# Optimization experiments

Measured on AMD Instinct MI355X. Metric: run time of the kernel, lower is better.

Reference implementation:

```python
import jax, jax.numpy as jnp
import numpy as np

EPS = 1e-5


def setup_inputs() -> dict:
    key = jax.random.key(0)
    ks = jax.random.split(key, 12)
    B, C, H, W = 1, 512, 64, 64
    d = C // 8
    inp = {
        "x": jax.random.normal(ks[0], (B, C, H, W), jnp.float32),
        "y": jax.random.normal(ks[1], (B, C, H, W), jnp.float32),
        "s_m": jax.random.uniform(ks[2], (H, W), jnp.float32),
        "q_m": jax.random.uniform(ks[3], (H, W), jnp.float32),
        "Wq": jax.random.normal(ks[4], (d, C), jnp.float32) * (1.0 / np.sqrt(C)),
        "bq": jnp.zeros((d,), jnp.float32),
        "Wk": jax.random.normal(ks[5], (d, C), jnp.float32) * (1.0 / np.sqrt(C)),
        "bk": jnp.zeros((d,), jnp.float32),
        "Wv": jax.random.normal(ks[6], (C, C), jnp.float32) * (1.0 / np.sqrt(C)),
        "bv": jnp.zeros((C,), jnp.float32),
        "W1": jax.random.normal(ks[7], (C, C), jnp.float32) * (1.0 / np.sqrt(C)),
        "b1": jnp.zeros((C,), jnp.float32),
        "W2": jax.random.normal(ks[8], (C, C), jnp.float32) * (1.0 / np.sqrt(C)),
        "b2": jnp.zeros((C,), jnp.float32),
        "gamma": jnp.ones((1, C, H, W), jnp.float32),
        "beta": jnp.zeros((1, C, H, W), jnp.float32),
    }
    return inp


def _conv1x1(x, Wt, b):
    # 1x1 Conv2d == per-pixel channel matmul
    return jnp.einsum("bchw,oc->bohw", x, Wt) + b[None, :, None, None]


def reference(x, y, s_m, q_m, Wq, bq, Wk, bk, Wv, bv, W1, b1, W2, b2, gamma, beta):
    B, C, H, W = x.shape
    N = H * W
    scale = (C // 8) ** (-0.5)

    q_m = jnp.where(q_m > 0.8, 1.0, 0.0).astype(x.dtype)
    x_fg = x * s_m[None, None]
    y_fg = y * q_m[None, None]

    def branch(q_in, k_in, v_in, use_max):
        q = _conv1x1(q_in, Wq, bq).reshape(B, -1, N).transpose(0, 2, 1) * scale  # [B,N,d]
        k = _conv1x1(k_in, Wk, bk).reshape(B, -1, N)                             # [B,d,N]
        v = _conv1x1(v_in, Wv, bv).reshape(B, -1, N)                             # [B,C,N]
        attn = jnp.einsum("bqd,bdk->bqk", q, k)                                  # [B,N,N]
        stat = jnp.max(attn) if use_max else jnp.min(attn)
        thr = (stat + jnp.mean(attn)) * 0.5
        attn = jnp.where(attn < thr, jnp.asarray(-999.0, attn.dtype), attn)
        attn = jax.nn.softmax(attn, axis=-1)
        out = jnp.einsum("bck,bqk->bcq", v, attn).reshape(B, C, H, W)
        h = out.transpose(0, 2, 3, 1)                                            # [B,H,W,C]
        h = jnp.maximum(h @ W1.T + b1, 0.0) @ W2.T + b2
        out = h.transpose(0, 3, 1, 2)
        # LayerNorm over all trailing dims [1,C,H,W] (B==1)
        mu = jnp.mean(out)
        var = jnp.mean((out - mu) ** 2)
        out = (out - mu) * jax.lax.rsqrt(var + EPS) * gamma + beta
        return out

    outx = branch(x_fg, y_fg, y_fg, True)
    outx = outx * s_m[None, None] + x * (1.0 - s_m)[None, None]
    outy = branch(y_fg, x, x, False)
    outy = outy * q_m[None, None] + y * (1.0 - q_m)[None, None]
    return outx, outy
```

## Files before the change

### kernel.cpp

```cpp
#include <hip/hip_runtime.h>
#include <math.h>

#define C_DIM 512
#define N_DIM 4096
#define CN (C_DIM * N_DIM)
#define SZO (N_DIM * C_DIM)
#define NN ((size_t)N_DIM * N_DIM)
#define NN_TOT ((long long)N_DIM * N_DIM)

typedef __attribute__((ext_vector_type(4))) float f32x4;
typedef __attribute__((ext_vector_type(8))) short short8;

__device__ __forceinline__ ushort f2bf(float f) {
    unsigned u = __float_as_uint(f);
    unsigned r = u + 0x7FFFu + ((u >> 16) & 1u);
    return (ushort)(r >> 16);
}
__device__ __forceinline__ float bf2f(ushort h) {
    return __uint_as_float((unsigned)h << 16);
}

__device__ __forceinline__ void gload16(const void* g, void* l) {
    __builtin_amdgcn_global_load_lds(
        (const __attribute__((address_space(1))) void*)g,
        (__attribute__((address_space(3))) void*)l, 16, 0, 0);
}

__global__ __launch_bounds__(256) void tconv64(
    const float* __restrict__ x, const float* __restrict__ y,
    ushort* __restrict__ xbT, ushort* __restrict__ ybT)
{
    const float* X = blockIdx.z ? y : x;
    ushort* XT = blockIdx.z ? ybT : xbT;
    __shared__ float t[64][65];
    const int c0 = blockIdx.x * 64;
    const int r0 = blockIdx.y * 64;
    const int ty = threadIdx.x >> 4, tx = threadIdx.x & 15;
    #pragma unroll
    for (int i = 0; i < 4; ++i) {
        int r = ty + i * 16;
        float4 v = *(const float4*)&X[(size_t)(r0 + r) * N_DIM + c0 + tx * 4];
        t[r][tx * 4 + 0] = v.x; t[r][tx * 4 + 1] = v.y;
        t[r][tx * 4 + 2] = v.z; t[r][tx * 4 + 3] = v.w;
    }
    __syncthreads();
    #pragma unroll
    for (int i = 0; i < 4; ++i) {
        int nn = ty + i * 16;
        ushort4 o;
        o.x = f2bf(t[tx * 4 + 0][nn]); o.y = f2bf(t[tx * 4 + 1][nn]);
        o.z = f2bf(t[tx * 4 + 2][nn]); o.w = f2bf(t[tx * 4 + 3][nn]);
        *(ushort4*)&XT[(size_t)(c0 + nn) * C_DIM + r0 + tx * 4] = o;
    }
}

__global__ __launch_bounds__(256) void cvtw3(
    const float* __restrict__ Wv, const float* __restrict__ W1,
    const float* __restrict__ W2, ushort* __restrict__ Wvb,
    ushort* __restrict__ W1b, ushort* __restrict__ W2b)
{
    const float* in  = (blockIdx.y == 0) ? Wv : (blockIdx.y == 1) ? W1 : W2;
    ushort*      out = (blockIdx.y == 0) ? Wvb : (blockIdx.y == 1) ? W1b : W2b;
    int i = (blockIdx.x * 256 + threadIdx.x) * 4;
    float4 v = *(const float4*)&in[i];
    ushort4 o = { f2bf(v.x), f2bf(v.y), f2bf(v.z), f2bf(v.w) };
    *(ushort4*)&out[i] = o;
}

template<int BM, int BN>
__global__ __launch_bounds__(256) void mfma_g(
    const ushort* __restrict__ A0, const ushort* __restrict__ A1,
    const ushort* __restrict__ B0, const ushort* __restrict__ B1,
    void* __restrict__ Out, size_t outBrStride,
    int M, int N, int K, int kLen, int nkz, int swapxy,
    const float* __restrict__ bias, int biasMode,
    const float* __restrict__ mask0, int mm0,
    const float* __restrict__ mask1, int mm1,
    int doRelu, int outBf16, float* __restrict__ lnp)
{
    constexpr int WAVES_M = BM / 64;
    constexpr int WAVES_N = 4 / WAVES_M;
    constexpr int WN = BN / WAVES_N;
    constexpr int FM = 4;
    constexpr int FN = WN / 16;
    constexpr int NCHUNK = (BM + BN) / 16;

    __shared__ ushort As[2][BM * 32];
    __shared__ ushort Bs[2][BN * 32];
    const int tid  = threadIdx.x;
    const int lane = tid & 63;
    const int wid  = tid >> 6;
    const int z  = blockIdx.z;
    const int br = z / nkz;
    const int kz = z % nkz;
    const ushort* A = br ? A1 : A0;
    const ushort* B = br ? B1 : B0;
    const float* mask = br ? mask1 : mask0;
    const int maskMode = br ? mm1 : mm0;

    const int bxm = swapxy ? blockIdx.x : blockIdx.y;
    const int bxn = swapxy ? blockIdx.y : blockIdx.x;
    const int m0 = bxm * BM, n0 = bxn * BN;
    const int wm = wid / WAVES_N, wn = wid % WAVES_N;
    const int wr = wm * 64, wc = wn * WN;
    const int kOff = kz * kLen;
    const int lrow = lane >> 2;
    const int kbl  = lane & 3;

    auto stage = [&](int buf, int t) {
        #pragma unroll
        for (int c = wid; c < NCHUNK; c += 4) {
            if (c < BM / 16) {
                int r = c * 16 + lrow;
                int kb = kbl ^ ((r >> 1) & 3);
                gload16(A + (size_t)(m0 + r) * K + kOff + t * 32 + kb * 8,
                        &As[buf][c * 512]);
            } else {
                int cb = c - BM / 16;
                int r = cb * 16 + lrow;
// ... 48 lines not shown
            for (int nc = 0; nc < FN; ++nc)
                #pragma unroll
                for (int j = 0; j < 4; ++j) {
                    int gm = m0 + wr + mr * 16 + orow + j;
                    int gn = n0 + wc + nc * 16 + ocol;
                    Of[(size_t)gm * N + gn] = acc[mr][nc][j];
                }
        return;
    }

    float mcol[FN], bcol[FN];
    #pragma unroll
    for (int nc = 0; nc < FN; ++nc) {
        int gn = n0 + wc + nc * 16 + ocol;
        mcol[nc] = (maskMode == 0) ? 1.0f
                 : (maskMode == 1) ? mask[gn]
                                   : (mask[gn] > 0.8f ? 1.0f : 0.0f);
        bcol[nc] = (biasMode == 2) ? bias[gn] : 0.0f;
    }
    ushort* Obf = (ushort*)Out + (size_t)br * outBrStride;
    float*  Of  = (float*)Out + (size_t)br * outBrStride;
    float lsum = 0.0f, lsq = 0.0f;
    #pragma unroll
    for (int mr = 0; mr < FM; ++mr) {
        #pragma unroll
        for (int j = 0; j < 4; ++j) {
            int gm = m0 + wr + mr * 16 + orow + j;
            float brow = (biasMode == 1) ? bias[gm] : 0.0f;
            #pragma unroll
            for (int nc = 0; nc < FN; ++nc) {
                int gn = n0 + wc + nc * 16 + ocol;
                float v = acc[mr][nc][j] * mcol[nc] + brow + bcol[nc];
                if (doRelu) v = fmaxf(v, 0.0f);
                if (outBf16) Obf[(size_t)gm * N + gn] = f2bf(v);
                else         Of[(size_t)gm * N + gn] = v;
                lsum += v; lsq = fmaf(v, v, lsq);
            }
        }
    }
    if (lnp) {
        __shared__ float redS[256], redQ[256];
        redS[tid] = lsum; redQ[tid] = lsq;
        __syncthreads();
        for (int s = 128; s > 0; s >>= 1) {
            if (tid < s) { redS[tid] += redS[tid + s]; redQ[tid] += redQ[tid + s]; }
            __syncthreads();
        }
        if (tid == 0) {
            int fb = blockIdx.y * gridDim.x + blockIdx.x;
            lnp[br * 512 + fb] = redS[0];
            lnp[br * 512 + 256 + fb] = redQ[0];
        }
    }
}

__global__ __launch_bounds__(256) void qkraw(
    const float* __restrict__ Wq, const float* __restrict__ Wk,
    const float* __restrict__ x, const float* __restrict__ y,
    float* __restrict__ PX)
{
    const int mt   = blockIdx.y & 1;
    const int srcT = blockIdx.y >> 1;
    const int kz   = blockIdx.z;
    const float* W = mt ? Wk : Wq;
    const float* X = srcT ? y : x;

    __shared__ float As[16][65];
    __shared__ float Bs[16][65];
    const int tid = threadIdx.x;
    const int n0 = blockIdx.x * 64;
    const int ty = tid >> 4, tx = tid & 15;
    float acc[4][4] = {};
    const int kbase = kz * 256;

    for (int k0 = kbase; k0 < kbase + 256; k0 += 16) {
        {
            int mm = tid >> 2, kq = (tid & 3) * 4;
            const float4 w4 = *(const float4*)&W[(size_t)mm * 512 + k0 + kq];
            As[kq + 0][mm] = w4.x; As[kq + 1][mm] = w4.y;
            As[kq + 2][mm] = w4.z; As[kq + 3][mm] = w4.w;
        }
        {
            int kk = tid >> 4, nq = (tid & 15) * 4;
            *(float4*)&Bs[kk][nq] = *(const float4*)&X[(size_t)(k0 + kk) * N_DIM + n0 + nq];
        }
        __syncthreads();
        #pragma unroll
        for (int kk = 0; kk < 16; ++kk) {
            float a[4], b[4];
            #pragma unroll
            for (int r = 0; r < 4; ++r) a[r] = As[kk][ty * 4 + r];
            #pragma unroll
            for (int c = 0; c < 4; ++c) b[c] = Bs[kk][tx * 4 + c];
            #pragma unroll
            for (int r = 0; r < 4; ++r)
                #pragma unroll
                for (int c = 0; c < 4; ++c)
                    acc[r][c] = fmaf(a[r], b[c], acc[r][c]);
        }
        __syncthreads();
    }
    float* dst = PX + ((size_t)(kz * 2 + srcT) * 128 + mt * 64) * N_DIM;
    #pragma unroll
    for (int r = 0; r < 4; ++r) {
        float4 o = make_float4(acc[r][0], acc[r][1], acc[r][2], acc[r][3]);
        *(float4*)&dst[(size_t)(ty * 4 + r) * N_DIM + n0 + tx * 4] = o;
    }
}

__global__ __launch_bounds__(256) void qkfinish(
    const float* __restrict__ PX,
    const float* __restrict__ s_m, const float* __restrict__ q_m,
    const float* __restrict__ bq, const float* __restrict__ bk,
    ushort* __restrict__ QF0, ushort* __restrict__ KF0,
    ushort* __restrict__ QF1, ushort* __restrict__ KF1)
{
    int gid = blockIdx.x * 256 + threadIdx.x;
    int lane = gid & 63;
    int rest = gid >> 6;
    int blk = rest & 255;
    int tensor = rest >> 8;
    int fr = lane & 15, quad = lane >> 4;
    int n = blk * 16 + fr;

    int srcT, rowbase, isQ;
    const float* bias;
    ushort* dst;
    float mv, scale;
    if (tensor == 0)      { srcT = 0; rowbase = 0;  isQ = 1; bias = bq; dst = QF0; scale = 0.125f; mv = s_m[n]; }
    else if (tensor == 1) { srcT = 1; rowbase = 64; isQ = 0; bias = bk; dst = KF0; scale = 1.0f;   mv = (q_m[n] > 0.8f) ? 1.0f : 0.0f; }
    else if (tensor == 2) { srcT = 1; rowbase = 0;  isQ = 1; bias = bq; dst = QF1; scale = 0.125f; mv = (q_m[n] > 0.8f) ? 1.0f : 0.0f; }
    else                  { srcT = 0; rowbase = 64; isQ = 0; bias = bk; dst = KF1; scale = 1.0f;   mv = 1.0f; }

    ushort hi0[8], lo0[8], hi1[8], lo1[8];
    #pragma unroll
    for (int j = 0; j < 8; ++j) {
        int d0 = quad * 8 + j, d1 = 32 + d0;
        float v0 = 0.0f, v1 = 0.0f;
        #pragma unroll
        for (int kz = 0; kz < 2; ++kz) {
            size_t base = ((size_t)(kz * 2 + srcT) * 128 + rowbase);
            v0 += PX[(base + d0) * N_DIM + n];
            v1 += PX[(base + d1) * N_DIM + n];
        }
        v0 = (v0 * mv + bias[d0]) * scale;
        v1 = (v1 * mv + bias[d1]) * scale;
        hi0[j] = f2bf(v0); lo0[j] = f2bf(v0 - bf2f(hi0[j]));
        hi1[j] = f2bf(v1); lo1[j] = f2bf(v1 - bf2f(hi1[j]));
    }
    auto wr8 = [&](int kstep, const ushort* v) {
        size_t base = ((size_t)(blk * 6 + kstep) * 64 + lane) * 8;
        *(ushort4*)&dst[base]     = *(const ushort4*)&v[0];
        *(ushort4*)&dst[base + 4] = *(const ushort4*)&v[4];
    };
    wr8(0, hi0); wr8(1, hi1);
    if (isQ) { wr8(2, hi0); wr8(3, hi1); wr8(4, lo0); wr8(5, lo1); }
    else     { wr8(2, lo0); wr8(3, lo1); wr8(4, hi0); wr8(5, hi1); }
}

__device__ __forceinline__ void scores_mfma(
    const ushort* __restrict__ QF, const ushort* __restrict__ KF,
    int m0, int n0, int wr, int wc, int lane, f32x4 acc[4][4])
{
    const int blkA0 = (m0 + wr) >> 4;
    const int blkB0 = (n0 + wc) >> 4;
    #pragma unroll
    for (int s = 0; s < 6; ++s) {
        short8 af[4], bf[4];
        #pragma unroll
        for (int mr = 0; mr < 4; ++mr)
            af[mr] = *(const short8*)&QF[((size_t)((blkA0 + mr) * 6 + s) * 64 + lane) * 8];
        #pragma unroll
        for (int nc = 0; nc < 4; ++nc)
            bf[nc] = *(const short8*)&KF[((size_t)((blkB0 + nc) * 6 + s) * 64 + lane) * 8];
        #pragma unroll
        for (int mr = 0; mr < 4; ++mr)
            #pragma unroll
            for (int nc = 0; nc < 4; ++nc)
                acc[mr][nc] = __builtin_amdgcn_mfma_f32_16x16x32_bf16(
                    af[mr], bf[nc], acc[mr][nc], 0, 0, 0);
    }
}

__global__ __launch_bounds__(256) void scores_pass1(
    const ushort* __restrict__ QF0, const ushort* __restrict__ KF0,
    const ushort* __restrict__ QF1, const ushort* __restrict__ KF1,
    float* __restrict__ part, float* __restrict__ rowmaxp)
{
    const int br = blockIdx.z;
    const ushort* QF = br ? QF1 : QF0;
    const ushort* KF = br ? KF1 : KF0;
    part    += (size_t)br * 3072;
    rowmaxp += (size_t)br * 131072;

    const int lane = threadIdx.x & 63, wid = threadIdx.x >> 6;
    const int m0 = blockIdx.y * 128, n0 = blockIdx.x * 128;
    const int wr = (wid >> 1) * 64, wc = (wid & 1) * 64;
    f32x4 acc[4][4] = {};
    scores_mfma(QF, KF, m0, n0, wr, wc, lane, acc);

    float lmax = -3.4e38f, lmin = 3.4e38f, lsum = 0.0f;
    float rmx[4][4];
    #pragma unroll
    for (int mr = 0; mr < 4; ++mr)
        #pragma unroll
        for (int j = 0; j < 4; ++j) rmx[mr][j] = -3.4e38f;
    #pragma unroll
    for (int mr = 0; mr < 4; ++mr)
        #pragma unroll
        for (int nc = 0; nc < 4; ++nc)
            #pragma unroll
            for (int j = 0; j < 4; ++j) {
                float v = acc[mr][nc][j];
                lsum += v; lmax = fmaxf(lmax, v); lmin = fminf(lmin, v);
                rmx[mr][j] = fmaxf(rmx[mr][j], v);
            }
    #pragma unroll
    for (int m = 1; m < 16; m <<= 1)
        #pragma unroll
        for (int mr = 0; mr < 4; ++mr)
            #pragma unroll
            for (int j = 0; j < 4; ++j)
                rmx[mr][j] = fmaxf(rmx[mr][j], __shfl_xor(rmx[mr][j], m, 64));

    __shared__ float wrm[2][128];
    const int orow = (lane >> 4) * 4;
    if ((lane & 15) == 0) {
        #pragma unroll
        for (int mr = 0; mr < 4; ++mr)
            #pragma unroll
            for (int j = 0; j < 4; ++j)
                wrm[wid & 1][wr + mr * 16 + orow + j] = rmx[mr][j];
    }
    __syncthreads();
    if (threadIdx.x < 128) {
        float v = fmaxf(wrm[0][threadIdx.x], wrm[1][threadIdx.x]);
        rowmaxp[(size_t)blockIdx.x * 4096 + m0 + threadIdx.x] = v;
    }

    __shared__ float red[256];
    const int tid = threadIdx.x;
    const int bid = blockIdx.y * 32 + blockIdx.x;
    __syncthreads();
    red[tid] = lmax; __syncthreads();
    for (int s = 128; s > 0; s >>= 1) { if (tid < s) red[tid] = fmaxf(red[tid], red[tid + s]); __syncthreads(); }
    if (tid == 0) part[bid] = red[0];
    __syncthreads();
    red[tid] = lmin; __syncthreads();
    for (int s = 128; s > 0; s >>= 1) { if (tid < s) red[tid] = fminf(red[tid], red[tid + s]); __syncthreads(); }
    if (tid == 0) part[1024 + bid] = red[0];
    __syncthreads();
    red[tid] = lsum; __syncthreads();
    for (int s = 128; s > 0; s >>= 1) { if (tid < s) red[tid] += red[tid + s]; __syncthreads(); }
    if (tid == 0) part[2048 + bid] = red[0];
}

__global__ __launch_bounds__(256) void stats_fin2(
    const float* __restrict__ part, float* __restrict__ stats)
{
    const int br = blockIdx.x;
    part += (size_t)br * 3072;
    __shared__ float rmax[256], rmin[256];
    __shared__ double rsum[256];
    int tid = threadIdx.x;
    float m1 = -3.4e38f, m2 = 3.4e38f; double s = 0.0;
    for (int i = tid; i < 1024; i += 256) {
        m1 = fmaxf(m1, part[i]);
        m2 = fminf(m2, part[1024 + i]);
        s += (double)part[2048 + i];
    }
    rmax[tid] = m1; rmin[tid] = m2; rsum[tid] = s;
    __syncthreads();
    for (int st = 128; st > 0; st >>= 1) {
        if (tid < st) {
            rmax[tid] = fmaxf(rmax[tid], rmax[tid + st]);
            rmin[tid] = fminf(rmin[tid], rmin[tid + st]);
            rsum[tid] += rsum[tid + st];
        }
        __syncthreads();
    }
    if (tid == 0) {
        float stat = (br == 0) ? rmax[0] : rmin[0];
        float mean = (float)(rsum[0] / (double)NN_TOT);
        stats[br] = 0.5f * (stat + mean);
    }
}

__global__ __launch_bounds__(256) void scores_pass2(
    const ushort* __restrict__ QF0, const ushort* __restrict__ KF0,
    const ushort* __restrict__ QF1, const ushort* __restrict__ KF1,
    const float* __restrict__ stats, const float* __restrict__ rowmaxp,
    ushort* __restrict__ Pe, float* __restrict__ rowsump)
{
    const int br = blockIdx.z;
    const ushort* QF = br ? QF1 : QF0;
    const ushort* KF = br ? KF1 : KF0;
    ushort* P = Pe + (size_t)br * NN;
    rowsump += (size_t)br * 131072;
    rowmaxp += (size_t)br * 131072;

    const int lane = threadIdx.x & 63, wid = threadIdx.x >> 6;
    const int m0 = blockIdx.y * 128, n0 = blockIdx.x * 128;
    const int wr = (wid >> 1) * 64, wc = (wid & 1) * 64;
    const float thr = stats[br];

    __shared__ float rowmL[128];
    if (threadIdx.x < 128) {
        int r = m0 + threadIdx.x;
        float m = -3.4e38f;
        #pragma unroll 8
        for (int b = 0; b < 32; ++b)
            m = fmaxf(m, rowmaxp[(size_t)b * 4096 + r]);
        rowmL[threadIdx.x] = (m >= thr) ? m : -1e30f;
    }
    __syncthreads();

    f32x4 acc[4][4] = {};
    scores_mfma(QF, KF, m0, n0, wr, wc, lane, acc);

    const int orow = (lane >> 4) * 4;
    const int ocol = lane & 15;
    float rm[4][4], rs[4][4];
    #pragma unroll
    for (int mr = 0; mr < 4; ++mr)
        #pragma unroll
        for (int j = 0; j < 4; ++j) {
            rm[mr][j] = rowmL[wr + mr * 16 + orow + j];
            rs[mr][j] = 0.0f;
        }
    #pragma unroll
    for (int mr = 0; mr < 4; ++mr)
        #pragma unroll
        for (int nc = 0; nc < 4; ++nc)
            #pragma unroll
            for (int j = 0; j < 4; ++j) {
                float s = acc[mr][nc][j];
                float m = rm[mr][j];
                float e = (s < thr) ? 0.0f : __expf(s - m);
                if (m < -1e29f) e = 1.0f;
                ushort h = f2bf(e);
                rs[mr][j] += bf2f(h);
                P[(size_t)(m0 + wr + mr * 16 + orow + j) * N_DIM
                  + n0 + wc + nc * 16 + ocol] = h;
            }
    #pragma unroll
    for (int m = 1; m < 16; m <<= 1)
        #pragma unroll
        for (int mr = 0; mr < 4; ++mr)
            #pragma unroll
            for (int j = 0; j < 4; ++j)
                rs[mr][j] += __shfl_xor(rs[mr][j], m, 64);

    __shared__ float wrs[2][128];
    if ((lane & 15) == 0) {
        #pragma unroll
        for (int mr = 0; mr < 4; ++mr)
            #pragma unroll
            for (int j = 0; j < 4; ++j)
                wrs[wid & 1][wr + mr * 16 + orow + j] = rs[mr][j];
    }
    __syncthreads();
    if (threadIdx.x < 128)
        rowsump[(size_t)blockIdx.x * 4096 + m0 + threadIdx.x] =
            wrs[0][threadIdx.x] + wrs[1][threadIdx.x];
}

__global__ __launch_bounds__(256) void reduce2row(
    const float* __restrict__ P4, const float* __restrict__ rowsump,
    ushort* __restrict__ O)
{
    const int br = blockIdx.y;
    const int tid = threadIdx.x;
    const int r0 = blockIdx.x * 2;
    __shared__ float invL[2];
    if (tid < 64) {
        int rw = tid >> 5, b = tid & 31;
        float s = rowsump[(size_t)br * 131072 + (size_t)b * 4096 + r0 + rw];
        #pragma unroll
        for (int m = 1; m < 32; m <<= 1) s += __shfl_xor(s, m, 64);
        if (b == 0) invL[rw] = 1.0f / s;
    }
    __syncthreads();
    int i = (blockIdx.x * 256 + tid) * 4;
    float sc = invL[(i >> 9) & 1];
    float4 a = *(const float4*)&P4[(size_t)(br * 2 + 0) * SZO + i];
    float4 b = *(const float4*)&P4[(size_t)(br * 2 + 1) * SZO + i];
    ushort4 o;
    o.x = f2bf((a.x + b.x) * sc);
    o.y = f2bf((a.y + b.y) * sc);
    o.z = f2bf((a.z + b.z) * sc);
    o.w = f2bf((a.w + b.w) * sc);
    *(ushort4*)&O[(size_t)br * SZO + i] = o;
}

__global__ __launch_bounds__(256) void gate_write(
    const float* __restrict__ H2, const float* __restrict__ lnp,
    const float* __restrict__ gamma, const float* __restrict__ beta,
    const float* __restrict__ x, const float* __restrict__ y,
    const float* __restrict__ s_m, const float* __restrict__ q_m,
    float* __restrict__ out)
{
    const int br = blockIdx.y;
    const int tid = threadIdx.x;
    __shared__ double rs[256], rq[256];
    rs[tid] = (double)lnp[(size_t)br * 512 + tid];
    rq[tid] = (double)lnp[(size_t)br * 512 + 256 + tid];
    __syncthreads();
    for (int st = 128; st > 0; st >>= 1) {
        if (tid < st) { rs[tid] += rs[tid + st]; rq[tid] += rq[tid + st]; }
        __syncthreads();
    }
    double muD = rs[0] / (double)CN;
    double varD = rq[0] / (double)CN - muD * muD;
    float mu = (float)muD;
    float rstd = (float)(1.0 / sqrt(varD + 1e-5));

    size_t i = ((size_t)blockIdx.x * 256 + tid) * 4;
// ... 16 lines not shown
    }
    float4 o; o.x = os[0]; o.y = os[1]; o.z = os[2]; o.w = os[3];
    *(float4*)&out[(size_t)br * CN + i] = o;
}

extern "C" void kernel_launch(void* const* d_in, const int* in_sizes, int n_in,
                              void* d_out, int out_size, void* d_ws, size_t ws_size,
                              hipStream_t stream)
{
    const float* x     = (const float*)d_in[0];
    const float* y     = (const float*)d_in[1];
    const float* s_m   = (const float*)d_in[2];
    const float* q_m   = (const float*)d_in[3];
    const float* Wq    = (const float*)d_in[4];
    const float* bq    = (const float*)d_in[5];
    const float* Wk    = (const float*)d_in[6];
    const float* bk    = (const float*)d_in[7];
    const float* Wv    = (const float*)d_in[8];
    const float* bv    = (const float*)d_in[9];
    const float* W1    = (const float*)d_in[10];
    const float* b1    = (const float*)d_in[11];
    const float* W2    = (const float*)d_in[12];
    const float* b2    = (const float*)d_in[13];
    const float* gamma = (const float*)d_in[14];
    const float* beta  = (const float*)d_in[15];
    float* out = (float*)d_out;

    float* ws = (float*)d_ws;
    float*  R1    = ws;
    float*  PX    = R1;
    float*  P4    = R1;
    ushort* QF0   = (ushort*)(R1 + 4194304);
    ushort* KF0   = QF0 + 786432;
    ushort* QF1   = KF0 + 786432;
    ushort* KF1   = QF1 + 786432;
    float*  SMALL = R1 + 8388608;
    float*  PART  = SMALL;
    float*  RMAXP = PART + 6144;
    float*  RSUMP = RMAXP + 262144;
    float*  LNP   = RSUMP + 262144;
    float*  STATS = LNP + 1024;
    ushort* Wvb   = (ushort*)(STATS + 64);
    ushort* W1b   = Wvb + 262144;
    ushort* W2b   = W1b + 262144;
    ushort* Vb    = W2b + 262144;
    ushort* R2    = Vb + 4194304;
    ushort* xbT   = R2;
    ushort* ybT   = R2 + 2097152;
    ushort* Pe    = R2;
    ushort* O1T   = R2;
    ushort* H1T   = R2 + 4194304;
    float*  H2    = (float*)(R2 + 8388608);

    tconv64<<<dim3(64, 8, 2), 256, 0, stream>>>(x, y, xbT, ybT);
    cvtw3<<<dim3(256, 3), 256, 0, stream>>>(Wv, W1, W2, Wvb, W1b, W2b);

    qkraw<<<dim3(64, 4, 2), 256, 0, stream>>>(Wq, Wk, x, y, PX);
    qkfinish<<<256, 256, 0, stream>>>(PX, s_m, q_m, bq, bk, QF0, KF0, QF1, KF1);

    mfma_g<64, 128><<<dim3(32, 8, 2), 256, 0, stream>>>(
        Wvb, Wvb, ybT, xbT, Vb, (size_t)CN,
        512, 4096, 512, 512, 1, 0, bv, 1, q_m, 2, nullptr, 0, 0, 1, nullptr);

    scores_pass1<<<dim3(32, 32, 2), 256, 0, stream>>>(QF0, KF0, QF1, KF1, PART, RMAXP);
    stats_fin2<<<2, 256, 0, stream>>>(PART, STATS);
    scores_pass2<<<dim3(32, 32, 2), 256, 0, stream>>>(QF0, KF0, QF1, KF1, STATS, RMAXP, Pe, RSUMP);

    mfma_g<64, 128><<<dim3(64, 4, 4), 256, 0, stream>>>(
        Pe, Pe + NN, Vb, Vb + CN, P4, 0,
        4096, 512, 4096, 2048, 2, 1, nullptr, 0, nullptr, 0, nullptr, 0, 0, 0, nullptr);
    reduce2row<<<dim3(2048, 2), 256, 0, stream>>>(P4, RSUMP, O1T);

    mfma_g<64, 64><<<dim3(64, 8, 2), 256, 0, stream>>>(
        O1T, O1T + SZO, W1b, W1b, H1T, (size_t)SZO,
        4096, 512, 512, 512, 1, 1, b1, 2, nullptr, 0, nullptr, 0, 1, 1, nullptr);

    mfma_g<64, 128><<<dim3(32, 8, 2), 256, 0, stream>>>(
        W2b, W2b, H1T, H1T + SZO, H2, (size_t)CN,
        512, 4096, 512, 512, 1, 0, b2, 1, nullptr, 0, nullptr, 0, 0, 0, LNP);

    gate_write<<<dim3(2048, 2), 256, 0, stream>>>(
        H2, LNP, gamma, beta, x, y, s_m, q_m, out);
}
```

Measured before the change: 255.9 us.

## Merge setup and projection kernels, fold stats reduction into pass2, enlarge GEMM tiles

Combines the transpose/convert, weight conversion and Q/K projection into one launch, with Q and K computed together so each x tile is loaded once. Fuses the V projection GEMM with scores pass1 in a single heterogeneous grid. Drops the separate stats kernel, so every pass2 block recomputes the global threshold from the partials. Raises the P·V and first FFN GEMM tiles to 128 rows. The goal is fewer launches, less idle tail time between small kernels and more reuse per tile. In exchange, pass2 blocks repeat the stats reduction and the bigger tiles yield fewer blocks.

```diff
diff --git a/kernel.cpp b/kernel.cpp
--- a/kernel.cpp
+++ b/kernel.cpp
@@ -26,45 +26,458 @@
         (__attribute__((address_space(3))) void*)l, 16, 0, 0);
 }
 
-__global__ __launch_bounds__(256) void tconv64(
+__global__ __launch_bounds__(256) void setup_all(
     const float* __restrict__ x, const float* __restrict__ y,
-    ushort* __restrict__ xbT, ushort* __restrict__ ybT)
-{
-    const float* X = blockIdx.z ? y : x;
-    ushort* XT = blockIdx.z ? ybT : xbT;
-    __shared__ float t[64][65];
-    const int c0 = blockIdx.x * 64;
-    const int r0 = blockIdx.y * 64;
-    const int ty = threadIdx.x >> 4, tx = threadIdx.x & 15;
-    #pragma unroll
-    for (int i = 0; i < 4; ++i) {
-        int r = ty + i * 16;
-        float4 v = *(const float4*)&X[(size_t)(r0 + r) * N_DIM + c0 + tx * 4];
-        t[r][tx * 4 + 0] = v.x; t[r][tx * 4 + 1] = v.y;
-        t[r][tx * 4 + 2] = v.z; t[r][tx * 4 + 3] = v.w;
-    }
-    __syncthreads();
-    #pragma unroll
-    for (int i = 0; i < 4; ++i) {
-        int nn = ty + i * 16;
-        ushort4 o;
-        o.x = f2bf(t[tx * 4 + 0][nn]); o.y = f2bf(t[tx * 4 + 1][nn]);
-        o.z = f2bf(t[tx * 4 + 2][nn]); o.w = f2bf(t[tx * 4 + 3][nn]);
-        *(ushort4*)&XT[(size_t)(c0 + nn) * C_DIM + r0 + tx * 4] = o;
-    }
-}
-
-__global__ __launch_bounds__(256) void cvtw3(
+    ushort* __restrict__ xbT, ushort* __restrict__ ybT,
     const float* __restrict__ Wv, const float* __restrict__ W1,
     const float* __restrict__ W2, ushort* __restrict__ Wvb,
-    ushort* __restrict__ W1b, ushort* __restrict__ W2b)
-{
-    const float* in  = (blockIdx.y == 0) ? Wv : (blockIdx.y == 1) ? W1 : W2;
-    ushort*      out = (blockIdx.y == 0) ? Wvb : (blockIdx.y == 1) ? W1b : W2b;
-    int i = (blockIdx.x * 256 + threadIdx.x) * 4;
-    float4 v = *(const float4*)&in[i];
-    ushort4 o = { f2bf(v.x), f2bf(v.y), f2bf(v.z), f2bf(v.w) };
-    *(ushort4*)&out[i] = o;
+    ushort* __restrict__ W1b, ushort* __restrict__ W2b,
+    const float* __restrict__ Wq, const float* __restrict__ Wk,
+    float* __restrict__ PX)
+{
+    __shared__ float t[64][65];
+    __shared__ float Asw[16][130];
+    __shared__ float Bsx[16][65];
+    const int id = blockIdx.x;
+    const int tid = threadIdx.x;
+
+    if (id < 1024) {
+        const int bx = id & 63, by = (id >> 6) & 7, bz = id >> 9;
+        const float* X = bz ? y : x;
+        ushort* XT = bz ? ybT : xbT;
+        const int c0 = bx * 64, r0 = by * 64;
+        const int ty = tid >> 4, tx = tid & 15;
+        #pragma unroll
+        for (int i = 0; i < 4; ++i) {
+            int r = ty + i * 16;
+            float4 v = *(const float4*)&X[(size_t)(r0 + r) * N_DIM + c0 + tx * 4];
+            t[r][tx * 4 + 0] = v.x; t[r][tx * 4 + 1] = v.y;
+            t[r][tx * 4 + 2] = v.z; t[r][tx * 4 + 3] = v.w;
+        }
+        __syncthreads();
+        #pragma unroll
+        for (int i = 0; i < 4; ++i) {
+            int nn = ty + i * 16;
+            ushort4 o;
+            o.x = f2bf(t[tx * 4 + 0][nn]); o.y = f2bf(t[tx * 4 + 1][nn]);
+            o.z = f2bf(t[tx * 4 + 2][nn]); o.w = f2bf(t[tx * 4 + 3][nn]);
+            *(ushort4*)&XT[(size_t)(c0 + nn) * C_DIM + r0 + tx * 4] = o;
+        }
+        return;
+    }
+    if (id < 1792) {
+        const int i2 = id - 1024;
+        const int bx = i2 & 255, by = i2 >> 8;
+        const float* in  = (by == 0) ? Wv : (by == 1) ? W1 : W2;
+        ushort*      out = (by == 0) ? Wvb : (by == 1) ? W1b : W2b;
+        int i = (bx * 256 + tid) * 4;
+        float4 v = *(const float4*)&in[i];
+        ushort4 o = { f2bf(v.x), f2bf(v.y), f2bf(v.z), f2bf(v.w) };
+        *(ushort4*)&out[i] = o;
+        return;
+    }
+    {
+        const int i3 = id - 1792;
+        const int ntile = i3 & 63;
+        const int srcT  = (i3 >> 6) & 1;
+        const int kz    = i3 >> 7;
+        const float* X = srcT ? y : x;
+        const int n0 = ntile * 64;
+        const int ty = tid >> 4, tx = tid & 15;
+        float accQ[4][4] = {}, accK[4][4] = {};
+        const int kbase = kz * 256;
+
+        for (int k0 = kbase; k0 < kbase + 256; k0 += 16) {
+            #pragma unroll
+            for (int i = 0; i < 2; ++i) {
+                int wi = tid + i * 256;
+                int mm = wi >> 2;
+                int kq = (wi & 3) * 4;
+                const float* Wp = (mm < 64) ? &Wq[(size_t)mm * 512]
+                                            : &Wk[(size_t)(mm - 64) * 512];
+                float4 w4 = *(const float4*)&Wp[k0 + kq];
+                Asw[kq + 0][mm] = w4.x; Asw[kq + 1][mm] = w4.y;
+                Asw[kq + 2][mm] = w4.z; Asw[kq + 3][mm] = w4.w;
+            }
+            {
+                int kk = tid >> 4, nq = (tid & 15) * 4;
+                *(float4*)&Bsx[kk][nq] = *(const float4*)&X[(size_t)(k0 + kk) * N_DIM + n0 + nq];
+            }
+            __syncthreads();
+            #pragma unroll
+            for (int kk = 0; kk < 16; ++kk) {
+                float aq[4], ak[4], b[4];
+                #pragma unroll
+                for (int r = 0; r < 4; ++r) { aq[r] = Asw[kk][ty * 4 + r]; ak[r] = Asw[kk][64 + ty * 4 + r]; }
+                #pragma unroll
+                for (int c = 0; c < 4; ++c) b[c] = Bsx[kk][tx * 4 + c];
+                #pragma unroll
+                for (int r = 0; r < 4; ++r)
+                    #pragma unroll
+                    for (int c = 0; c < 4; ++c) {
+                        accQ[r][c] = fmaf(aq[r], b[c], accQ[r][c]);
+                        accK[r][c] = fmaf(ak[r], b[c], accK[r][c]);
+                    }
+            }
+            __syncthreads();
+        }
+        float* dst = PX + ((size_t)(kz * 2 + srcT) * 128) * N_DIM;
+        #pragma unroll
+        for (int r = 0; r < 4; ++r) {
+            float4 oq = make_float4(accQ[r][0], accQ[r][1], accQ[r][2], accQ[r][3]);
+            *(float4*)&dst[(size_t)(ty * 4 + r) * N_DIM + n0 + tx * 4] = oq;
+            float4 ok = make_float4(accK[r][0], accK[r][1], accK[r][2], accK[r][3]);
+            *(float4*)&dst[(size_t)(64 + ty * 4 + r) * N_DIM + n0 + tx * 4] = ok;
+        }
+    }
+}
+
+__global__ __launch_bounds__(256) void qkfinish(
+    const float* __restrict__ PX,
+    const float* __restrict__ s_m, const float* __restrict__ q_m,
+    const float* __restrict__ bq, const float* __restrict__ bk,
+    ushort* __restrict__ QF0, ushort* __restrict__ KF0,
+    ushort* __restrict__ QF1, ushort* __restrict__ KF1)
+{
+    int gid = blockIdx.x * 256 + threadIdx.x;
+    int lane = gid & 63;
+    int rest = gid >> 6;
+    int blk = rest & 255;
+    int tensor = rest >> 8;
+    int fr = lane & 15, quad = lane >> 4;
+    int n = blk * 16 + fr;
+
+    int srcT, rowbase, isQ;
+    const float* bias;
+    ushort* dst;
+    float mv, scale;
+    if (tensor == 0)      { srcT = 0; rowbase = 0;  isQ = 1; bias = bq; dst = QF0; scale = 0.125f; mv = s_m[n]; }
+    else if (tensor == 1) { srcT = 1; rowbase = 64; isQ = 0; bias = bk; dst = KF0; scale = 1.0f;   mv = (q_m[n] > 0.8f) ? 1.0f : 0.0f; }
+    else if (tensor == 2) { srcT = 1; rowbase = 0;  isQ = 1; bias = bq; dst = QF1; scale = 0.125f; mv = (q_m[n] > 0.8f) ? 1.0f : 0.0f; }
+    else                  { srcT = 0; rowbase = 64; isQ = 0; bias = bk; dst = KF1; scale = 1.0f;   mv = 1.0f; }
+
+    ushort hi0[8], lo0[8], hi1[8], lo1[8];
+    #pragma unroll
+    for (int j = 0; j < 8; ++j) {
+        int d0 = quad * 8 + j, d1 = 32 + d0;
+        float v0 = 0.0f, v1 = 0.0f;
+        #pragma unroll
+        for (int kz = 0; kz < 2; ++kz) {
+            size_t base = ((size_t)(kz * 2 + srcT) * 128 + rowbase);
+            v0 += PX[(base + d0) * N_DIM + n];
+            v1 += PX[(base + d1) * N_DIM + n];
+        }
+        v0 = (v0 * mv + bias[d0]) * scale;
+        v1 = (v1 * mv + bias[d1]) * scale;
+        hi0[j] = f2bf(v0); lo0[j] = f2bf(v0 - bf2f(hi0[j]));
+        hi1[j] = f2bf(v1); lo1[j] = f2bf(v1 - bf2f(hi1[j]));
+    }
+    auto wr8 = [&](int kstep, const ushort* v) {
+        size_t base = ((size_t)(blk * 6 + kstep) * 64 + lane) * 8;
+        *(ushort4*)&dst[base]     = *(const ushort4*)&v[0];
+        *(ushort4*)&dst[base + 4] = *(const ushort4*)&v[4];
+    };
+    wr8(0, hi0); wr8(1, hi1);
+    if (isQ) { wr8(2, hi0); wr8(3, hi1); wr8(4, lo0); wr8(5, lo1); }
+    else     { wr8(2, lo0); wr8(3, lo1); wr8(4, hi0); wr8(5, hi1); }
+}
+
+__device__ __forceinline__ void scores_mfma(
+    const ushort* __restrict__ QF, const ushort* __restrict__ KF,
+    int m0, int n0, int wr, int wc, int lane, f32x4 acc[4][4])
+{
+    const int blkA0 = (m0 + wr) >> 4;
+    const int blkB0 = (n0 + wc) >> 4;
+    #pragma unroll
+    for (int s = 0; s < 6; ++s) {
+        short8 af[4], bf[4];
+        #pragma unroll
+        for (int mr = 0; mr < 4; ++mr)
+            af[mr] = *(const short8*)&QF[((size_t)((blkA0 + mr) * 6 + s) * 64 + lane) * 8];
+        #pragma unroll
+        for (int nc = 0; nc < 4; ++nc)
+            bf[nc] = *(const short8*)&KF[((size_t)((blkB0 + nc) * 6 + s) * 64 + lane) * 8];
+        #pragma unroll
+        for (int mr = 0; mr < 4; ++mr)
+            #pragma unroll
+            for (int nc = 0; nc < 4; ++nc)
+                acc[mr][nc] = __builtin_amdgcn_mfma_f32_16x16x32_bf16(
+                    af[mr], bf[nc], acc[mr][nc], 0, 0, 0);
+    }
+}
+
+__global__ __launch_bounds__(256) void vproj_p1(
+    const ushort* __restrict__ Wvb,
+    const ushort* __restrict__ xbT, const ushort* __restrict__ ybT,
+    const float* __restrict__ bv, const float* __restrict__ q_m,
+    ushort* __restrict__ Vb,
+    const ushort* __restrict__ QF0, const ushort* __restrict__ KF0,
+    const ushort* __restrict__ QF1, const ushort* __restrict__ KF1,
+    float* __restrict__ part, float* __restrict__ rowmaxp)
+{
+    __shared__ ushort As[2][128 * 32];
+    __shared__ ushort Bs[2][128 * 32];
+    __shared__ float wrm[2][128];
+    __shared__ float red[256];
+    const int id = blockIdx.x;
+    const int tid = threadIdx.x;
+    const int lane = tid & 63;
+    const int wid  = tid >> 6;
+
+    if (id < 256) {
+        const int bxn = id & 31;
+        const int bym = (id >> 5) & 3;
+        const int br  = id >> 7;
+        const ushort* A = Wvb;
+        const ushort* B = br ? xbT : ybT;
+        const int m0 = bym * 128, n0 = bxn * 128;
+        const int wr = (wid >> 1) * 64, wc = (wid & 1) * 64;
+        const int lrow = lane >> 2;
+        const int kbl  = lane & 3;
+        const int K = 512;
+
+        auto stage = [&](int buf, int t) {
+            #pragma unroll
+            for (int c = wid; c < 16; c += 4) {
+                if (c < 8) {
+                    int r = c * 16 + lrow;
+                    int kb = kbl ^ ((r >> 1) & 3);
+                    gload16(A + (size_t)(m0 + r) * K + t * 32 + kb * 8, &As[buf][c * 512]);
+                } else {
+                    int cb = c - 8;
+                    int r = cb * 16 + lrow;
+                    int kb = kbl ^ ((r >> 1) & 3);
+                    gload16(B + (size_t)(n0 + r) * K + t * 32 + kb * 8, &Bs[buf][cb * 512]);
+                }
+            }
+        };
+
+        f32x4 acc[4][4] = {};
+        const int fr = lane & 15;
+        const int kq = lane >> 4;
+        stage(0, 0);
+        asm volatile("s_waitcnt vmcnt(0)" ::: "memory");
+        __syncthreads();
+        int cur = 0;
+        for (int t = 0; t < 16; ++t) {
+            if (t + 1 < 16) stage(cur ^ 1, t + 1);
+            short8 af[4], bf[4];
+            #pragma unroll
+            for (int mr = 0; mr < 4; ++mr) {
+                int rA = wr + mr * 16 + fr;
+                af[mr] = *(const short8*)&As[cur][rA * 32 + (kq ^ ((rA >> 1) & 3)) * 8];
+            }
+            #pragma unroll
+            for (int nc = 0; nc < 4; ++nc) {
+                int rB = wc + nc * 16 + fr;
+                bf[nc] = *(const short8*)&Bs[cur][rB * 32 + (kq ^ ((rB >> 1) & 3)) * 8];
+            }
+            #pragma unroll
+            for (int mr = 0; mr < 4; ++mr)
+                #pragma unroll
+                for (int nc = 0; nc < 4; ++nc)
+                    acc[mr][nc] = __builtin_amdgcn_mfma_f32_16x16x32_bf16(
+                        af[mr], bf[nc], acc[mr][nc], 0, 0, 0);
+            asm volatile("s_waitcnt vmcnt(0)" ::: "memory");
+            __syncthreads();
+            cur ^= 1;
+        }
+        const int orow = (lane >> 4) * 4;
+        const int ocol = lane & 15;
+        float mcol[4];
+        #pragma unroll
+        for (int nc = 0; nc < 4; ++nc) {
+            int gn = n0 + wc + nc * 16 + ocol;
+            mcol[nc] = br ? 1.0f : ((q_m[gn] > 0.8f) ? 1.0f : 0.0f);
+        }
+        ushort* Obf = Vb + (size_t)br * CN;
+        #pragma unroll
+        for (int mr = 0; mr < 4; ++mr)
+            #pragma unroll
+            for (int j = 0; j < 4; ++j) {
+                int gm = m0 + wr + mr * 16 + orow + j;
+                float brow = bv[gm];
+                #pragma unroll
+                for (int nc = 0; nc < 4; ++nc) {
+                    int gn = n0 + wc + nc * 16 + ocol;
+                    float v = acc[mr][nc][j] * mcol[nc] + brow;
+                    Obf[(size_t)gm * N_DIM + gn] = f2bf(v);
+                }
+            }
+        return;
+    }
+
+    {
+        const int p = id - 256;
+        const int bxn = p & 31;
+        const int bym = (p >> 5) & 31;
+        const int br  = p >> 10;
+        const ushort* QF = br ? QF1 : QF0;
+        const ushort* KF = br ? KF1 : KF0;
+        float* pt = part + (size_t)br * 3072;
+        float* rmp = rowmaxp + (size_t)br * 131072;
+
+        const int m0 = bym * 128, n0 = bxn * 128;
+        const int wr = (wid >> 1) * 64, wc = (wid & 1) * 64;
+        f32x4 acc[4][4] = {};
+        scores_mfma(QF, KF, m0, n0, wr, wc, lane, acc);
+
+        float lmax = -3.4e38f, lmin = 3.4e38f, lsum = 0.0f;
+        float rmx[4][4];
+        #pragma unroll
+        for (int mr = 0; mr < 4; ++mr)
+            #pragma unroll
+            for (int j = 0; j < 4; ++j) rmx[mr][j] = -3.4e38f;
+        #pragma unroll
+        for (int mr = 0; mr < 4; ++mr)
+            #pragma unroll
+            for (int nc = 0; nc < 4; ++nc)
+                #pragma unroll
+                for (int j = 0; j < 4; ++j) {
+                    float v = acc[mr][nc][j];
+                    lsum += v; lmax = fmaxf(lmax, v); lmin = fminf(lmin, v);
+                    rmx[mr][j] = fmaxf(rmx[mr][j], v);
+                }
+        #pragma unroll
+        for (int m = 1; m < 16; m <<= 1)
+            #pragma unroll
+            for (int mr = 0; mr < 4; ++mr)
+                #pragma unroll
+                for (int j = 0; j < 4; ++j)
+                    rmx[mr][j] = fmaxf(rmx[mr][j], __shfl_xor(rmx[mr][j], m, 64));
+
+        const int orow = (lane >> 4) * 4;
+        if ((lane & 15) == 0) {
+            #pragma unroll
+            for (int mr = 0; mr < 4; ++mr)
+                #pragma unroll
+                for (int j = 0; j < 4; ++j)
+                    wrm[wid & 1][wr + mr * 16 + orow + j] = rmx[mr][j];
+        }
+        __syncthreads();
+        if (tid < 128) {
+            float v = fmaxf(wrm[0][tid], wrm[1][tid]);
+            rmp[(size_t)bxn * 4096 + m0 + tid] = v;
+        }
+
+        const int bid = bym * 32 + bxn;
+        __syncthreads();
+        red[tid] = lmax; __syncthreads();
+        for (int s = 128; s > 0; s >>= 1) { if (tid < s) red[tid] = fmaxf(red[tid], red[tid + s]); __syncthreads(); }
+        if (tid == 0) pt[bid] = red[0];
+        __syncthreads();
+        red[tid] = lmin; __syncthreads();
+        for (int s = 128; s > 0; s >>= 1) { if (tid < s) red[tid] = fminf(red[tid], red[tid + s]); __syncthreads(); }
+        if (tid == 0) pt[1024 + bid] = red[0];
+        __syncthreads();
+        red[tid] = lsum; __syncthreads();
+        for (int s = 128; s > 0; s >>= 1) { if (tid < s) red[tid] += red[tid + s]; __syncthreads(); }
+        if (tid == 0) pt[2048 + bid] = red[0];
+    }
+}
+
+__global__ __launch_bounds__(256) void scores_pass2(
+    const ushort* __restrict__ QF0, const ushort* __restrict__ KF0,
+    const ushort* __restrict__ QF1, const ushort* __restrict__ KF1,
+    const float* __restrict__ part, const float* __restrict__ rowmaxp,
+    ushort* __restrict__ Pe, float* __restrict__ rowsump)
+{
+    const int br = blockIdx.z;
+    const ushort* QF = br ? QF1 : QF0;
+    const ushort* KF = br ? KF1 : KF0;
+    ushort* P = Pe + (size_t)br * NN;
+    rowsump += (size_t)br * 131072;
+    rowmaxp += (size_t)br * 131072;
+    const float* pp = part + (size_t)br * 3072;
+
+    const int tid = threadIdx.x;
+    const int lane = tid & 63, wid = tid >> 6;
+    const int m0 = blockIdx.y * 128, n0 = blockIdx.x * 128;
+    const int wr = (wid >> 1) * 64, wc = (wid & 1) * 64;
+
+    __shared__ float smx[256], smn[256];
+    __shared__ double ssm[256];
+    {
+        float m1 = -3.4e38f, m2 = 3.4e38f; double s = 0.0;
+        for (int i = tid; i < 1024; i += 256) {
+            m1 = fmaxf(m1, pp[i]);
+            m2 = fminf(m2, pp[1024 + i]);
+            s += (double)pp[2048 + i];
+        }
+        smx[tid] = m1; smn[tid] = m2; ssm[tid] = s;
+        __syncthreads();
+        for (int st = 128; st > 0; st >>= 1) {
+            if (tid < st) {
+                smx[tid] = fmaxf(smx[tid], smx[tid + st]);
+                smn[tid] = fminf(smn[tid], smn[tid + st]);
+                ssm[tid] += ssm[tid + st];
+            }
+            __syncthreads();
+        }
+    }
+    const float stat = (br == 0) ? smx[0] : smn[0];
+    const float mean = (float)(ssm[0] / (double)NN_TOT);
+    const float thr = 0.5f * (stat + mean);
+
+    __shared__ float rowmL[128];
+    if (tid < 128) {
+        int r = m0 + tid;
+        float m = -3.4e38f;
+        #pragma unroll 8
+        for (int b = 0; b < 32; ++b)
+            m = fmaxf(m, rowmaxp[(size_t)b * 4096 + r]);
+        rowmL[tid] = (m >= thr) ? m : -1e30f;
+    }
+    __syncthreads();
+
+    f32x4 acc[4][4] = {};
+    scores_mfma(QF, KF, m0, n0, wr, wc, lane, acc);
+
+    const int orow = (lane >> 4) * 4;
+    const int ocol = lane & 15;
+    float rm[4][4], rs[4][4];
+    #pragma unroll
+    for (int mr = 0; mr < 4; ++mr)
+        #pragma unroll
+        for (int j = 0; j < 4; ++j) {
+            rm[mr][j] = rowmL[wr + mr * 16 + orow + j];
+            rs[mr][j] = 0.0f;
+        }
+    #pragma unroll
+    for (int mr = 0; mr < 4; ++mr)
+        #pragma unroll
+        for (int nc = 0; nc < 4; ++nc)
+            #pragma unroll
+            for (int j = 0; j < 4; ++j) {
+                float s = acc[mr][nc][j];
+                float m = rm[mr][j];
+                float e = (s < thr) ? 0.0f : __expf(s - m);
+                if (m < -1e29f) e = 1.0f;
+                ushort h = f2bf(e);
+                rs[mr][j] += bf2f(h);
+                P[(size_t)(m0 + wr + mr * 16 + orow + j) * N_DIM
+                  + n0 + wc + nc * 16 + ocol] = h;
+            }
+    #pragma unroll
+    for (int m = 1; m < 16; m <<= 1)
+        #pragma unroll
+        for (int mr = 0; mr < 4; ++mr)
+            #pragma unroll
+            for (int j = 0; j < 4; ++j)
+                rs[mr][j] += __shfl_xor(rs[mr][j], m, 64);
+
+    __shared__ float wrs[2][128];
+    if ((lane & 15) == 0) {
+        #pragma unroll
+        for (int mr = 0; mr < 4; ++mr)
+            #pragma unroll
+            for (int j = 0; j < 4; ++j)
+                wrs[wid & 1][wr + mr * 16 + orow + j] = rs[mr][j];
+    }
+    __syncthreads();
+    if (tid < 128)
+        rowsump[(size_t)blockIdx.x * 4096 + m0 + tid] =
+            wrs[0][tid] + wrs[1][tid];
 }
 
 template<int BM, int BN>
@@ -219,317 +632,6 @@
             lnp[br * 512 + 256 + fb] = redQ[0];
         }
     }
-}
-
-__global__ __launch_bounds__(256) void qkraw(
-    const float* __restrict__ Wq, const float* __restrict__ Wk,
-    const float* __restrict__ x, const float* __restrict__ y,
-    float* __restrict__ PX)
-{
-    const int mt   = blockIdx.y & 1;
-    const int srcT = blockIdx.y >> 1;
-    const int kz   = blockIdx.z;
-    const float* W = mt ? Wk : Wq;
-    const float* X = srcT ? y : x;
-
-    __shared__ float As[16][65];
-    __shared__ float Bs[16][65];
-    const int tid = threadIdx.x;
-    const int n0 = blockIdx.x * 64;
-    const int ty = tid >> 4, tx = tid & 15;
-    float acc[4][4] = {};
-    const int kbase = kz * 256;
-
-    for (int k0 = kbase; k0 < kbase + 256; k0 += 16) {
-        {
-            int mm = tid >> 2, kq = (tid & 3) * 4;
-            const float4 w4 = *(const float4*)&W[(size_t)mm * 512 + k0 + kq];
-            As[kq + 0][mm] = w4.x; As[kq + 1][mm] = w4.y;
-            As[kq + 2][mm] = w4.z; As[kq + 3][mm] = w4.w;
-        }
-        {
-            int kk = tid >> 4, nq = (tid & 15) * 4;
-            *(float4*)&Bs[kk][nq] = *(const float4*)&X[(size_t)(k0 + kk) * N_DIM + n0 + nq];
-        }
-        __syncthreads();
-        #pragma unroll
-        for (int kk = 0; kk < 16; ++kk) {
-            float a[4], b[4];
-            #pragma unroll
-            for (int r = 0; r < 4; ++r) a[r] = As[kk][ty * 4 + r];
-            #pragma unroll
-            for (int c = 0; c < 4; ++c) b[c] = Bs[kk][tx * 4 + c];
-            #pragma unroll
-            for (int r = 0; r < 4; ++r)
-                #pragma unroll
-                for (int c = 0; c < 4; ++c)
-                    acc[r][c] = fmaf(a[r], b[c], acc[r][c]);
-        }
-        __syncthreads();
-    }
-    float* dst = PX + ((size_t)(kz * 2 + srcT) * 128 + mt * 64) * N_DIM;
-    #pragma unroll
-    for (int r = 0; r < 4; ++r) {
-        float4 o = make_float4(acc[r][0], acc[r][1], acc[r][2], acc[r][3]);
-        *(float4*)&dst[(size_t)(ty * 4 + r) * N_DIM + n0 + tx * 4] = o;
-    }
-}
-
-__global__ __launch_bounds__(256) void qkfinish(
-    const float* __restrict__ PX,
-    const float* __restrict__ s_m, const float* __restrict__ q_m,
-    const float* __restrict__ bq, const float* __restrict__ bk,
-    ushort* __restrict__ QF0, ushort* __restrict__ KF0,
-    ushort* __restrict__ QF1, ushort* __restrict__ KF1)
-{
-    int gid = blockIdx.x * 256 + threadIdx.x;
-    int lane = gid & 63;
-    int rest = gid >> 6;
-    int blk = rest & 255;
-    int tensor = rest >> 8;
-    int fr = lane & 15, quad = lane >> 4;
-    int n = blk * 16 + fr;
-
-    int srcT, rowbase, isQ;
-    const float* bias;
-    ushort* dst;
-    float mv, scale;
-    if (tensor == 0)      { srcT = 0; rowbase = 0;  isQ = 1; bias = bq; dst = QF0; scale = 0.125f; mv = s_m[n]; }
-    else if (tensor == 1) { srcT = 1; rowbase = 64; isQ = 0; bias = bk; dst = KF0; scale = 1.0f;   mv = (q_m[n] > 0.8f) ? 1.0f : 0.0f; }
-    else if (tensor == 2) { srcT = 1; rowbase = 0;  isQ = 1; bias = bq; dst = QF1; scale = 0.125f; mv = (q_m[n] > 0.8f) ? 1.0f : 0.0f; }
-    else                  { srcT = 0; rowbase = 64; isQ = 0; bias = bk; dst = KF1; scale = 1.0f;   mv = 1.0f; }
-
-    ushort hi0[8], lo0[8], hi1[8], lo1[8];
-    #pragma unroll
-    for (int j = 0; j < 8; ++j) {
-        int d0 = quad * 8 + j, d1 = 32 + d0;
-        float v0 = 0.0f, v1 = 0.0f;
-        #pragma unroll
-        for (int kz = 0; kz < 2; ++kz) {
-            size_t base = ((size_t)(kz * 2 + srcT) * 128 + rowbase);
-            v0 += PX[(base + d0) * N_DIM + n];
-            v1 += PX[(base + d1) * N_DIM + n];
-        }
-        v0 = (v0 * mv + bias[d0]) * scale;
-        v1 = (v1 * mv + bias[d1]) * scale;
-        hi0[j] = f2bf(v0); lo0[j] = f2bf(v0 - bf2f(hi0[j]));
-        hi1[j] = f2bf(v1); lo1[j] = f2bf(v1 - bf2f(hi1[j]));
-    }
-    auto wr8 = [&](int kstep, const ushort* v) {
-        size_t base = ((size_t)(blk * 6 + kstep) * 64 + lane) * 8;
-        *(ushort4*)&dst[base]     = *(const ushort4*)&v[0];
-        *(ushort4*)&dst[base + 4] = *(const ushort4*)&v[4];
-    };
-    wr8(0, hi0); wr8(1, hi1);
-    if (isQ) { wr8(2, hi0); wr8(3, hi1); wr8(4, lo0); wr8(5, lo1); }
-    else     { wr8(2, lo0); wr8(3, lo1); wr8(4, hi0); wr8(5, hi1); }
-}
-
-__device__ __forceinline__ void scores_mfma(
-    const ushort* __restrict__ QF, const ushort* __restrict__ KF,
-    int m0, int n0, int wr, int wc, int lane, f32x4 acc[4][4])
-{
-    const int blkA0 = (m0 + wr) >> 4;
-    const int blkB0 = (n0 + wc) >> 4;
-    #pragma unroll
-    for (int s = 0; s < 6; ++s) {
-        short8 af[4], bf[4];
-        #pragma unroll
-        for (int mr = 0; mr < 4; ++mr)
-            af[mr] = *(const short8*)&QF[((size_t)((blkA0 + mr) * 6 + s) * 64 + lane) * 8];
-        #pragma unroll
-        for (int nc = 0; nc < 4; ++nc)
-            bf[nc] = *(const short8*)&KF[((size_t)((blkB0 + nc) * 6 + s) * 64 + lane) * 8];
-        #pragma unroll
-        for (int mr = 0; mr < 4; ++mr)
-            #pragma unroll
-            for (int nc = 0; nc < 4; ++nc)
-                acc[mr][nc] = __builtin_amdgcn_mfma_f32_16x16x32_bf16(
-                    af[mr], bf[nc], acc[mr][nc], 0, 0, 0);
-    }
-}
-
-__global__ __launch_bounds__(256) void scores_pass1(
-    const ushort* __restrict__ QF0, const ushort* __restrict__ KF0,
-    const ushort* __restrict__ QF1, const ushort* __restrict__ KF1,
-    float* __restrict__ part, float* __restrict__ rowmaxp)
-{
-    const int br = blockIdx.z;
-    const ushort* QF = br ? QF1 : QF0;
-    const ushort* KF = br ? KF1 : KF0;
-    part    += (size_t)br * 3072;
-    rowmaxp += (size_t)br * 131072;
-
-    const int lane = threadIdx.x & 63, wid = threadIdx.x >> 6;
-    const int m0 = blockIdx.y * 128, n0 = blockIdx.x * 128;
-    const int wr = (wid >> 1) * 64, wc = (wid & 1) * 64;
-    f32x4 acc[4][4] = {};
-    scores_mfma(QF, KF, m0, n0, wr, wc, lane, acc);
-
-    float lmax = -3.4e38f, lmin = 3.4e38f, lsum = 0.0f;
-    float rmx[4][4];
-    #pragma unroll
-    for (int mr = 0; mr < 4; ++mr)
-        #pragma unroll
-        for (int j = 0; j < 4; ++j) rmx[mr][j] = -3.4e38f;
-    #pragma unroll
-    for (int mr = 0; mr < 4; ++mr)
-        #pragma unroll
-        for (int nc = 0; nc < 4; ++nc)
-            #pragma unroll
-            for (int j = 0; j < 4; ++j) {
-                float v = acc[mr][nc][j];
-                lsum += v; lmax = fmaxf(lmax, v); lmin = fminf(lmin, v);
-                rmx[mr][j] = fmaxf(rmx[mr][j], v);
-            }
-    #pragma unroll
-    for (int m = 1; m < 16; m <<= 1)
-        #pragma unroll
-        for (int mr = 0; mr < 4; ++mr)
-            #pragma unroll
-            for (int j = 0; j < 4; ++j)
-                rmx[mr][j] = fmaxf(rmx[mr][j], __shfl_xor(rmx[mr][j], m, 64));
-
-    __shared__ float wrm[2][128];
-    const int orow = (lane >> 4) * 4;
-    if ((lane & 15) == 0) {
-        #pragma unroll
-        for (int mr = 0; mr < 4; ++mr)
-            #pragma unroll
-            for (int j = 0; j < 4; ++j)
-                wrm[wid & 1][wr + mr * 16 + orow + j] = rmx[mr][j];
-    }
-    __syncthreads();
-    if (threadIdx.x < 128) {
-        float v = fmaxf(wrm[0][threadIdx.x], wrm[1][threadIdx.x]);
-        rowmaxp[(size_t)blockIdx.x * 4096 + m0 + threadIdx.x] = v;
-    }
-
-    __shared__ float red[256];
-    const int tid = threadIdx.x;
-    const int bid = blockIdx.y * 32 + blockIdx.x;
-    __syncthreads();
-    red[tid] = lmax; __syncthreads();
-    for (int s = 128; s > 0; s >>= 1) { if (tid < s) red[tid] = fmaxf(red[tid], red[tid + s]); __syncthreads(); }
-    if (tid == 0) part[bid] = red[0];
-    __syncthreads();
-    red[tid] = lmin; __syncthreads();
-    for (int s = 128; s > 0; s >>= 1) { if (tid < s) red[tid] = fminf(red[tid], red[tid + s]); __syncthreads(); }
-    if (tid == 0) part[1024 + bid] = red[0];
-    __syncthreads();
-    red[tid] = lsum; __syncthreads();
-    for (int s = 128; s > 0; s >>= 1) { if (tid < s) red[tid] += red[tid + s]; __syncthreads(); }
-    if (tid == 0) part[2048 + bid] = red[0];
-}
-
-__global__ __launch_bounds__(256) void stats_fin2(
-    const float* __restrict__ part, float* __restrict__ stats)
-{
-    const int br = blockIdx.x;
-    part += (size_t)br * 3072;
-    __shared__ float rmax[256], rmin[256];
-    __shared__ double rsum[256];
-    int tid = threadIdx.x;
-    float m1 = -3.4e38f, m2 = 3.4e38f; double s = 0.0;
-    for (int i = tid; i < 1024; i += 256) {
-        m1 = fmaxf(m1, part[i]);
-        m2 = fminf(m2, part[1024 + i]);
-        s += (double)part[2048 + i];
-    }
-    rmax[tid] = m1; rmin[tid] = m2; rsum[tid] = s;
-    __syncthreads();
-    for (int st = 128; st > 0; st >>= 1) {
-        if (tid < st) {
-            rmax[tid] = fmaxf(rmax[tid], rmax[tid + st]);
-            rmin[tid] = fminf(rmin[tid], rmin[tid + st]);
-            rsum[tid] += rsum[tid + st];
-        }
-        __syncthreads();
-    }
-    if (tid == 0) {
-        float stat = (br == 0) ? rmax[0] : rmin[0];
-        float mean = (float)(rsum[0] / (double)NN_TOT);
-        stats[br] = 0.5f * (stat + mean);
-    }
-}
-
-__global__ __launch_bounds__(256) void scores_pass2(
-    const ushort* __restrict__ QF0, const ushort* __restrict__ KF0,
-    const ushort* __restrict__ QF1, const ushort* __restrict__ KF1,
-    const float* __restrict__ stats, const float* __restrict__ rowmaxp,
-    ushort* __restrict__ Pe, float* __restrict__ rowsump)
-{
-    const int br = blockIdx.z;
-    const ushort* QF = br ? QF1 : QF0;
-    const ushort* KF = br ? KF1 : KF0;
-    ushort* P = Pe + (size_t)br * NN;
-    rowsump += (size_t)br * 131072;
-    rowmaxp += (size_t)br * 131072;
-
-    const int lane = threadIdx.x & 63, wid = threadIdx.x >> 6;
-    const int m0 = blockIdx.y * 128, n0 = blockIdx.x * 128;
-    const int wr = (wid >> 1) * 64, wc = (wid & 1) * 64;
-    const float thr = stats[br];
-
-    __shared__ float rowmL[128];
-    if (threadIdx.x < 128) {
-        int r = m0 + threadIdx.x;
-        float m = -3.4e38f;
-        #pragma unroll 8
-        for (int b = 0; b < 32; ++b)
-            m = fmaxf(m, rowmaxp[(size_t)b * 4096 + r]);
-        rowmL[threadIdx.x] = (m >= thr) ? m : -1e30f;
-    }
-    __syncthreads();
-
-    f32x4 acc[4][4] = {};
-    scores_mfma(QF, KF, m0, n0, wr, wc, lane, acc);
-
-    const int orow = (lane >> 4) * 4;
-    const int ocol = lane & 15;
-    float rm[4][4], rs[4][4];
-    #pragma unroll
-    for (int mr = 0; mr < 4; ++mr)
-        #pragma unroll
-        for (int j = 0; j < 4; ++j) {
-            rm[mr][j] = rowmL[wr + mr * 16 + orow + j];
-            rs[mr][j] = 0.0f;
-        }
-    #pragma unroll
-    for (int mr = 0; mr < 4; ++mr)
-        #pragma unroll
-        for (int nc = 0; nc < 4; ++nc)
-            #pragma unroll
-            for (int j = 0; j < 4; ++j) {
-                float s = acc[mr][nc][j];
-                float m = rm[mr][j];
-                float e = (s < thr) ? 0.0f : __expf(s - m);
-                if (m < -1e29f) e = 1.0f;
-                ushort h = f2bf(e);
-                rs[mr][j] += bf2f(h);
-                P[(size_t)(m0 + wr + mr * 16 + orow + j) * N_DIM
-                  + n0 + wc + nc * 16 + ocol] = h;
-            }
-    #pragma unroll
-    for (int m = 1; m < 16; m <<= 1)
-        #pragma unroll
-        for (int mr = 0; mr < 4; ++mr)
-            #pragma unroll
-            for (int j = 0; j < 4; ++j)
-                rs[mr][j] += __shfl_xor(rs[mr][j], m, 64);
-
-    __shared__ float wrs[2][128];
-    if ((lane & 15) == 0) {
-        #pragma unroll
-        for (int mr = 0; mr < 4; ++mr)
-            #pragma unroll
-            for (int j = 0; j < 4; ++j)
-                wrs[wid & 1][wr + mr * 16 + orow + j] = rs[mr][j];
-    }
-    __syncthreads();
-    if (threadIdx.x < 128)
-        rowsump[(size_t)blockIdx.x * 4096 + m0 + threadIdx.x] =
-            wrs[0][threadIdx.x] + wrs[1][threadIdx.x];
 }
 
 __global__ __launch_bounds__(256) void reduce2row(
@@ -652,26 +754,24 @@
     ushort* H1T   = R2 + 4194304;
     float*  H2    = (float*)(R2 + 8388608);
 
-    tconv64<<<dim3(64, 8, 2), 256, 0, stream>>>(x, y, xbT, ybT);
-    cvtw3<<<dim3(256, 3), 256, 0, stream>>>(Wv, W1, W2, Wvb, W1b, W2b);
-
-    qkraw<<<dim3(64, 4, 2), 256, 0, stream>>>(Wq, Wk, x, y, PX);
+    setup_all<<<2048, 256, 0, stream>>>(
+        x, y, xbT, ybT, Wv, W1, W2, Wvb, W1b, W2b, Wq, Wk, PX);
+
     qkfinish<<<256, 256, 0, stream>>>(PX, s_m, q_m, bq, bk, QF0, KF0, QF1, KF1);
 
-    mfma_g<64, 128><<<dim3(32, 8, 2), 256, 0, stream>>>(
-        Wvb, Wvb, ybT, xbT, Vb, (size_t)CN,
-        512, 4096, 512, 512, 1, 0, bv, 1, q_m, 2, nullptr, 0, 0, 1, nullptr);
-
-    scores_pass1<<<dim3(32, 32, 2), 256, 0, stream>>>(QF0, KF0, QF1, KF1, PART, RMAXP);
-    stats_fin2<<<2, 256, 0, stream>>>(PART, STATS);
-    scores_pass2<<<dim3(32, 32, 2), 256, 0, stream>>>(QF0, KF0, QF1, KF1, STATS, RMAXP, Pe, RSUMP);
-
-    mfma_g<64, 128><<<dim3(64, 4, 4), 256, 0, stream>>>(
+    vproj_p1<<<2304, 256, 0, stream>>>(
+        Wvb, xbT, ybT, bv, q_m, Vb, QF0, KF0, QF1, KF1, PART, RMAXP);
+
+    scores_pass2<<<dim3(32, 32, 2), 256, 0, stream>>>(
+        QF0, KF0, QF1, KF1, PART, RMAXP, Pe, RSUMP);
+
+    mfma_g<128, 128><<<dim3(32, 4, 4), 256, 0, stream>>>(
         Pe, Pe + NN, Vb, Vb + CN, P4, 0,
         4096, 512, 4096, 2048, 2, 1, nullptr, 0, nullptr, 0, nullptr, 0, 0, 0, nullptr);
+
     reduce2row<<<dim3(2048, 2), 256, 0, stream>>>(P4, RSUMP, O1T);
 
-    mfma_g<64, 64><<<dim3(64, 8, 2), 256, 0, stream>>>(
+    mfma_g<128, 64><<<dim3(32, 8, 2), 256, 0, stream>>>(
         O1T, O1T + SZO, W1b, W1b, H1T, (size_t)SZO,
         4096, 512, 512, 512, 1, 1, b1, 2, nullptr, 0, nullptr, 0, 1, 1, nullptr);
 
```

New measurement: 303.0 us. 18.4% more time.
